# Optimization experiments

Measured on AMD Instinct MI355X. Metric: run time of the kernel, lower is better.

## Reference

```python
import jax, jax.numpy as jnp
import numpy as np

C = 512
GROUPS = 8
EPS = 1e-5


def setup_inputs() -> dict:
    key = jax.random.key(0)
    ks = jax.random.split(key, 7)
    b, c, h, w = 32, C, 32, 32
    x = jax.random.normal(ks[0], (b, c, h, w), dtype=jnp.float32)
    norm_gamma = jnp.ones((c,), dtype=jnp.float32)
    norm_beta = jnp.zeros((c,), dtype=jnp.float32)
    # 1x1 convs == per-pixel linear layers; store as [out, in] matrices
    qkv_w = jax.random.normal(ks[1], (3 * c, c), dtype=jnp.float32) * (1.0 / np.sqrt(c))
    qkv_b = jnp.zeros((3 * c,), dtype=jnp.float32)
    out_w = jax.random.normal(ks[2], (c, c), dtype=jnp.float32) * (1.0 / np.sqrt(c))
    out_b = jnp.zeros((c,), dtype=jnp.float32)
    return {"x": x, "norm_gamma": norm_gamma, "norm_beta": norm_beta,
            "qkv_w": qkv_w, "qkv_b": qkv_b, "out_w": out_w, "out_b": out_b}


def group_norm(x, gamma, beta):
    b, c, h, w = x.shape
    xg = x.reshape(b, GROUPS, c // GROUPS, h, w)
    mean = jnp.mean(xg, axis=(2, 3, 4), keepdims=True)
    var = jnp.var(xg, axis=(2, 3, 4), keepdims=True)
    xg = (xg - mean) * jax.lax.rsqrt(var + EPS)
    x = xg.reshape(b, c, h, w)
    return x * gamma[None, :, None, None] + beta[None, :, None, None]


def reference(x, norm_gamma, norm_beta, qkv_w, qkv_b, out_w, out_b):
    b, c, h, w = x.shape
    xn = group_norm(x, norm_gamma, norm_beta)
    # 1x1 conv: [b,c,h,w] -> [b,3c,h,w]
    qkv = jnp.einsum('oc,bchw->bohw', qkv_w, xn) + qkv_b[None, :, None, None]
    q, k, v = jnp.split(qkv.reshape(b, 3 * c, h * w), 3, axis=1)  # each [b,c,hw]
    scale = c ** (-0.5)
    attn = jnp.einsum('bci,bcj->bij', q, k) * scale  # [b, hw, hw]
    attn = jax.nn.softmax(attn, axis=-1)
    out = jnp.einsum('bij,bcj->bci', attn, v).reshape(b, c, h, w)
    out = jnp.einsum('oc,bchw->bohw', out_w, out) + out_b[None, :, None, None]
    return x + out
```

## Files before the change

### kernel.cpp

```cpp
#include <hip/hip_runtime.h>

#define HW 1024
#define CD 512

typedef __bf16 bf16x8 __attribute__((ext_vector_type(8)));
typedef float f32x4 __attribute__((ext_vector_type(4)));

__device__ __forceinline__ unsigned short f2bf(float f) {
    unsigned int u = __float_as_uint(f);
    u += 0x7fff + ((u >> 16) & 1);
    return (unsigned short)(u >> 16);
}
__device__ __forceinline__ float bf2f(unsigned short h) {
    return __uint_as_float((unsigned)h << 16);
}

#define AS1(p) ((__attribute__((address_space(1))) void*)(p))
#define AS3(p) ((__attribute__((address_space(3))) void*)(p))
#define GLD16(gp, lp) __builtin_amdgcn_global_load_lds(AS1(gp), AS3(lp), 16, 0, 0)
#define WAITVM(n) do { asm volatile("s_waitcnt vmcnt(" #n ")" ::: "memory"); \
                       __builtin_amdgcn_sched_barrier(0); } while (0)

__global__ __launch_bounds__(256)
void gn_stats(const float* __restrict__ x, float* __restrict__ mean, float* __restrict__ rstd) {
    int bg = blockIdx.x;
    const float4* p4 = (const float4*)(x + (size_t)bg * 65536);
    int tid = threadIdx.x;
    float s = 0.f, ss = 0.f;
#pragma unroll 8
    for (int it = 0; it < 64; ++it) {
        float4 v = p4[tid + it * 256];
        s  += v.x + v.y + v.z + v.w;
        ss += v.x * v.x + v.y * v.y + v.z * v.z + v.w * v.w;
    }
#pragma unroll
    for (int d = 32; d > 0; d >>= 1) { s += __shfl_down(s, d); ss += __shfl_down(ss, d); }
    __shared__ float ls[4], lss[4];
    if ((tid & 63) == 0) { ls[tid >> 6] = s; lss[tid >> 6] = ss; }
    __syncthreads();
    if (tid == 0) {
        float S = ls[0] + ls[1] + ls[2] + ls[3];
        float SS = lss[0] + lss[1] + lss[2] + lss[3];
        float m = S * (1.f / 65536.f);
        float v = SS * (1.f / 65536.f) - m * m;
        mean[bg] = m;
        rstd[bg] = rsqrtf(v + 1e-5f);
    }
}

__global__ __launch_bounds__(256)
void gn_norm_t(const float* __restrict__ x, const float* __restrict__ mean, const float* __restrict__ rstd,
               const float* __restrict__ gamma, const float* __restrict__ beta,
               unsigned short* __restrict__ xnT) {
    __shared__ unsigned short tile[64][67];
    int i0 = blockIdx.x * 64, c0 = blockIdx.y * 64, b = blockIdx.z;
    float m = mean[b * 8 + blockIdx.y];
    float r = rstd[b * 8 + blockIdx.y];
    int tid = threadIdx.x;
    int tr = tid >> 4, tc = (tid & 15) * 4;
    const float* xb = x + ((size_t)b * CD + c0) * HW + i0;
#pragma unroll
    for (int p = 0; p < 4; ++p) {
        int c = tr + p * 16;
        float g = gamma[c0 + c] * r;
        float bb = beta[c0 + c] - m * g;
        float4 v = *(const float4*)(xb + (size_t)c * HW + tc);
        tile[c][tc + 0] = f2bf(v.x * g + bb);
        tile[c][tc + 1] = f2bf(v.y * g + bb);
        tile[c][tc + 2] = f2bf(v.z * g + bb);
        tile[c][tc + 3] = f2bf(v.w * g + bb);
    }
    __syncthreads();
    unsigned short* ob = xnT + ((size_t)b * HW + i0) * CD + c0;
#pragma unroll
    for (int p = 0; p < 4; ++p) {
        int ir = tr + p * 16;
        ushort4 u;
        u.x = tile[tc + 0][ir];
        u.y = tile[tc + 1][ir];
        u.z = tile[tc + 2][ir];
        u.w = tile[tc + 3][ir];
        *(ushort4*)(ob + (size_t)ir * CD + tc) = u;
    }
}

__global__ __launch_bounds__(256)
void tpose3_bf16(const float* __restrict__ qkv_w, unsigned short* __restrict__ dst0) {
    __shared__ unsigned short tile[64][67];
    const int zmap[3] = {0, 2, 1};
    const float* src = qkv_w + (size_t)blockIdx.z * CD * CD;
    unsigned short* dst = dst0 + (size_t)zmap[blockIdx.z] * CD * CD;
    int i0 = blockIdx.x * 64, c0 = blockIdx.y * 64;
    int tid = threadIdx.x;
    int tr = tid >> 4, tc = (tid & 15) * 4;
#pragma unroll
    for (int p = 0; p < 4; ++p) {
        int r = tr + p * 16;
        float4 v = *(const float4*)(src + (size_t)(i0 + r) * CD + c0 + tc);
        tile[r][tc + 0] = f2bf(v.x);
        tile[r][tc + 1] = f2bf(v.y);
        tile[r][tc + 2] = f2bf(v.z);
        tile[r][tc + 3] = f2bf(v.w);
    }
    __syncthreads();
#pragma unroll
    for (int p = 0; p < 4; ++p) {
        int ir = tr + p * 16;
        ushort4 u;
        u.x = tile[tc + 0][ir];
        u.y = tile[tc + 1][ir];
        u.z = tile[tc + 2][ir];
        u.w = tile[tc + 3][ir];
        *(ushort4*)(dst + (size_t)(c0 + ir) * CD + i0 + tc) = u;
    }
}

__global__ __launch_bounds__(256)
void cvt_bf16(const float* __restrict__ src, unsigned short* __restrict__ dst) {
    int i = blockIdx.x * 256 + threadIdx.x;
    float4 v = ((const float4*)src)[i];
    ushort4 u;
    u.x = f2bf(v.x); u.y = f2bf(v.y); u.z = f2bf(v.z); u.w = f2bf(v.w);
    ((ushort4*)dst)[i] = u;
}

__global__ __launch_bounds__(256)
void gvec_kernel(const float* __restrict__ wk, const float* __restrict__ bq,
                 float* __restrict__ g) {
    __shared__ float red[4][64];
    int d = blockIdx.x * 64 + (threadIdx.x & 63);
    int os = threadIdx.x >> 6;
    float acc = 0.f;
    for (int o = os * 128; o < os * 128 + 128; ++o)
        acc += wk[(size_t)o * CD + d] * bq[o];
    red[os][threadIdx.x & 63] = acc;
    __syncthreads();
    if (threadIdx.x < 64)
        g[blockIdx.x * 64 + threadIdx.x] = red[0][threadIdx.x] + red[1][threadIdx.x] +
                                           red[2][threadIdx.x] + red[3][threadIdx.x];
}

__global__ __launch_bounds__(256)
void bias2_kernel(const float* __restrict__ out_w, const float* __restrict__ bv,
                  float* __restrict__ bias2) {
    int wid = threadIdx.x >> 6, lane = threadIdx.x & 63;
    int o = blockIdx.x * 4 + wid;
    float acc = 0.f;
#pragma unroll
    for (int t = 0; t < 512; t += 64)
        acc += out_w[(size_t)o * CD + t + lane] * bv[t + lane];
#pragma unroll
    for (int d = 32; d > 0; d >>= 1) acc += __shfl_down(acc, d);
    if (lane == 0) bias2[o] = acc;
}

template<int EPI>
__global__ __launch_bounds__(512, 2)
void gemm8(const unsigned short* __restrict__ A, const unsigned short* __restrict__ B,
           unsigned short* __restrict__ C, const float* __restrict__ bias,
           int M, int N, int K, long long sA, long long sB, long long sC) {
    unsigned nx = gridDim.x, ny = gridDim.y;
    unsigned lin = blockIdx.x + nx * (blockIdx.y + ny * blockIdx.z);
    unsigned nwg = nx * ny * gridDim.z;
    unsigned work = (lin & 7) * (nwg >> 3) + (lin >> 3);
    unsigned bx = work % nx; work /= nx;
    unsigned by = work % ny;
    unsigned bz = work / ny;

    A += (size_t)bz * sA;
    B += (size_t)bz * sB;
    int m0 = by * 256, n0 = bx * 256;

    __shared__ unsigned short lA[2][256 * 64];
    __shared__ unsigned short lB[2][256 * 64];

    int tid = threadIdx.x, lane = tid & 63, wid = tid >> 6;
    int wr = wid >> 2, wc = wid & 3;

    f32x4 acc[8][4] = {};

    int strow[4], stcol[4];
#pragma unroll
    for (int s = 0; s < 4; ++s) {
        int idx = s * 512 + tid;
        strow[s] = idx >> 3;
        stcol[s] = ((idx & 7) ^ (strow[s] & 7)) * 8;
    }

    auto stage = [&](int buf, int kt) {
        int k0 = kt << 6;
#pragma unroll
        for (int s = 0; s < 4; ++s)
            GLD16(A + (size_t)(m0 + strow[s]) * K + k0 + stcol[s], &lA[buf][(size_t)(s * 512 + tid) * 8]);
#pragma unroll
        for (int s = 0; s < 4; ++s)
            GLD16(B + (size_t)(n0 + strow[s]) * K + k0 + stcol[s], &lB[buf][(size_t)(s * 512 + tid) * 8]);
    };

    int NT = K >> 6;
    stage(0, 0);
    if (NT > 1) stage(1, 1);

    for (int t = 0; t < NT; ++t) {
        if (t < NT - 1) WAITVM(8); else WAITVM(0);
        __builtin_amdgcn_s_barrier();
        const char* pa = (const char*)lA[t & 1];
        const char* pb = (const char*)lB[t & 1];
        __builtin_amdgcn_s_setprio(1);
#pragma unroll
        for (int kk = 0; kk < 64; kk += 32) {
            int koff = (kk + (lane >> 4) * 8) * 2;
            bf16x8 af[8], bfr[4];
#pragma unroll
            for (int m = 0; m < 8; ++m) {
                int row = wr * 128 + m * 16 + (lane & 15);
                af[m] = *(const bf16x8*)(pa + ((row * 128 + koff) ^ ((row & 7) << 4)));
            }
#pragma unroll
            for (int n = 0; n < 4; ++n) {
                int row = wc * 64 + n * 16 + (lane & 15);
                bfr[n] = *(const bf16x8*)(pb + ((row * 128 + koff) ^ ((row & 7) << 4)));
            }
#pragma unroll
            for (int m = 0; m < 8; ++m)
#pragma unroll
                for (int n = 0; n < 4; ++n)
                    acc[m][n] = __builtin_amdgcn_mfma_f32_16x16x32_bf16(af[m], bfr[n], acc[m][n], 0, 0, 0);
        }
        __builtin_amdgcn_s_setprio(0);
        __builtin_amdgcn_s_barrier();
        if (t + 2 < NT) stage(t & 1, t + 2);
    }

    int rl = (lane >> 4) * 4;
    int cl = lane & 15;
    unsigned short* Cb = C + (size_t)bz * sC;
#pragma unroll
    for (int m = 0; m < 8; ++m)
#pragma unroll
        for (int n = 0; n < 4; ++n) {
            int gm = m0 + wr * 128 + m * 16 + rl;
            int gn = n0 + wc * 64 + n * 16 + cl;
#pragma unroll
            for (int rg = 0; rg < 4; ++rg) {
                float v = acc[m][n][rg];
                if (EPI == 0) v += bias[gn];
                if (EPI == 1) v += bias[gm + rg];
                Cb[(size_t)(gm + rg) * N + gn] = f2bf(v);
            }
        }
}

__global__ __launch_bounds__(512, 2)
void scores8(const unsigned short* __restrict__ T1, const unsigned short* __restrict__ xnT,
             unsigned short* __restrict__ S, float* __restrict__ tmax, float* __restrict__ tsum) {
    unsigned nx = gridDim.x, ny = gridDim.y;
    unsigned lin = blockIdx.x + nx * (blockIdx.y + ny * blockIdx.z);
    unsigned nwg = nx * ny * gridDim.z;
    unsigned work = (lin & 7) * (nwg >> 3) + (lin >> 3);
    unsigned bx = work % nx; work /= nx;
    unsigned by = work % ny;
    unsigned bz = work / ny;

    const unsigned short* Ab = T1 + (size_t)bz * HW * CD;
    const unsigned short* Bb = xnT + (size_t)bz * HW * CD;
    int m0 = by * 256, n0 = bx * 256;

    __shared__ unsigned short lA[2][256 * 64];
    __shared__ unsigned short lB[2][256 * 64];
    __shared__ float redm[4][256];
    __shared__ float reds[4][256];

    int tid = threadIdx.x, lane = tid & 63, wid = tid >> 6;
    int wr = wid >> 2, wc = wid & 3;

    f32x4 acc[8][4] = {};

    int strow[4], stcol[4];
#pragma unroll
    for (int s = 0; s < 4; ++s) {
        int idx = s * 512 + tid;
        strow[s] = idx >> 3;
        stcol[s] = ((idx & 7) ^ (strow[s] & 7)) * 8;
    }

    auto stage = [&](int buf, int kt) {
        int k0 = kt << 6;
#pragma unroll
        for (int s = 0; s < 4; ++s)
            GLD16(Ab + (size_t)(m0 + strow[s]) * CD + k0 + stcol[s], &lA[buf][(size_t)(s * 512 + tid) * 8]);
#pragma unroll
        for (int s = 0; s < 4; ++s)
            GLD16(Bb + (size_t)(n0 + strow[s]) * CD + k0 + stcol[s], &lB[buf][(size_t)(s * 512 + tid) * 8]);
    };

    stage(0, 0);
    stage(1, 1);

    for (int t = 0; t < 8; ++t) {
        if (t < 7) WAITVM(8); else WAITVM(0);
        __builtin_amdgcn_s_barrier();
        const char* pa = (const char*)lA[t & 1];
        const char* pb = (const char*)lB[t & 1];
        __builtin_amdgcn_s_setprio(1);
#pragma unroll
        for (int kk = 0; kk < 64; kk += 32) {
            int koff = (kk + (lane >> 4) * 8) * 2;
            bf16x8 af[8], bfr[4];
#pragma unroll
            for (int m = 0; m < 8; ++m) {
                int row = wr * 128 + m * 16 + (lane & 15);
                af[m] = *(const bf16x8*)(pa + ((row * 128 + koff) ^ ((row & 7) << 4)));
            }
#pragma unroll
            for (int n = 0; n < 4; ++n) {
                int row = wc * 64 + n * 16 + (lane & 15);
                bfr[n] = *(const bf16x8*)(pb + ((row * 128 + koff) ^ ((row & 7) << 4)));
            }
#pragma unroll
            for (int m = 0; m < 8; ++m)
#pragma unroll
                for (int n = 0; n < 4; ++n)
                    acc[m][n] = __builtin_amdgcn_mfma_f32_16x16x32_bf16(af[m], bfr[n], acc[m][n], 0, 0, 0);
        }
        __builtin_amdgcn_s_setprio(0);
        __builtin_amdgcn_s_barrier();
        if (t + 2 < 8) stage(t & 1, t + 2);
    }

    const float SL2E = 0.044194173824159216f * 1.4426950408889634f;
#pragma unroll
    for (int m = 0; m < 8; ++m)
#pragma unroll
        for (int n = 0; n < 4; ++n) acc[m][n] *= SL2E;

    int rl = (lane >> 4) * 4;
    int cl = lane & 15;

    float mr[8][4];
#pragma unroll
    for (int m = 0; m < 8; ++m)
#pragma unroll
        for (int rg = 0; rg < 4; ++rg)
            mr[m][rg] = fmaxf(fmaxf(acc[m][0][rg], acc[m][1][rg]),
                              fmaxf(acc[m][2][rg], acc[m][3][rg]));
#pragma unroll
    for (int d = 1; d < 16; d <<= 1)
#pragma unroll
        for (int m = 0; m < 8; ++m)
#pragma unroll
            for (int rg = 0; rg < 4; ++rg) mr[m][rg] = fmaxf(mr[m][rg], __shfl_xor(mr[m][rg], d));
    if ((lane & 15) == 0)
#pragma unroll
        for (int m = 0; m < 8; ++m)
#pragma unroll
            for (int rg = 0; rg < 4; ++rg) redm[wc][wr * 128 + m * 16 + rl + rg] = mr[m][rg];
    __syncthreads();
    float Mt[8][4];
#pragma unroll
    for (int m = 0; m < 8; ++m)
#pragma unroll
        for (int rg = 0; rg < 4; ++rg) {
            int row = wr * 128 + m * 16 + rl + rg;
            Mt[m][rg] = fmaxf(fmaxf(redm[0][row], redm[1][row]),
                              fmaxf(redm[2][row], redm[3][row]));
        }

    float sr[8][4] = {};
#pragma unroll
    for (int m = 0; m < 8; ++m)
#pragma unroll
        for (int n = 0; n < 4; ++n)
#pragma unroll
            for (int rg = 0; rg < 4; ++rg) {
                float e = __builtin_amdgcn_exp2f(acc[m][n][rg] - Mt[m][rg]);
                acc[m][n][rg] = e;
                sr[m][rg] += e;
            }
#pragma unroll
    for (int d = 1; d < 16; d <<= 1)
#pragma unroll
        for (int m = 0; m < 8; ++m)
#pragma unroll
            for (int rg = 0; rg < 4; ++rg) sr[m][rg] += __shfl_xor(sr[m][rg], d);
    if ((lane & 15) == 0)
#pragma unroll
        for (int m = 0; m < 8; ++m)
#pragma unroll
            for (int rg = 0; rg < 4; ++rg) reds[wc][wr * 128 + m * 16 + rl + rg] = sr[m][rg];
    __syncthreads();

    if (tid < 256) {
        float M = fmaxf(fmaxf(redm[0][tid], redm[1][tid]),
                        fmaxf(redm[2][tid], redm[3][tid]));
        float Z = reds[0][tid] + reds[1][tid] + reds[2][tid] + reds[3][tid];
        size_t o = ((size_t)bz * 4 + bx) * HW + m0 + tid;
        tmax[o] = M;
        tsum[o] = Z;
    }

    unsigned short* Sb = S + (size_t)bz * HW * HW;
#pragma unroll
    for (int m = 0; m < 8; ++m)
#pragma unroll
        for (int n = 0; n < 4; ++n) {
            int gm = m0 + wr * 128 + m * 16 + rl;
            int gn = n0 + wc * 64 + n * 16 + cl;
#pragma unroll
            for (int rg = 0; rg < 4; ++rg)
                Sb[(size_t)(gm + rg) * HW + gn] = f2bf(acc[m][n][rg]);
        }
}

template<int EPI>
__global__ __launch_bounds__(256, 2)
void gemm_bt(const unsigned short* __restrict__ A, const unsigned short* __restrict__ B,
             void* __restrict__ Cv, const float* __restrict__ bias,
             int M, int N, int K, long long sA, long long sB, long long sC) {
    unsigned nx = gridDim.x, ny = gridDim.y;
    unsigned lin = blockIdx.x + nx * (blockIdx.y + ny * blockIdx.z);
    unsigned nwg = nx * ny * gridDim.z;
    unsigned work = (lin & 7) * (nwg >> 3) + (lin >> 3);
    unsigned bx = work % nx; work /= nx;
    unsigned by = work % ny;
    unsigned bz = work / ny;

    A += (size_t)bz * sA;
    B += (size_t)bz * sB;
    int m0 = by * 128, n0 = bx * 128;

    __shared__ unsigned short lA[2][128 * 64];
    __shared__ unsigned short lB[2][128 * 64];

    int tid = threadIdx.x;
    int lane = tid & 63;
    int wr = (tid >> 6) >> 1, wc = (tid >> 6) & 1;

    f32x4 acc[4][4] = {};

    int strow[4], stcol[4];
#pragma unroll
    for (int s = 0; s < 4; ++s) {
        int row = (s * 256 + tid) >> 3;
        int g = (tid & 7) ^ (row & 7);
        strow[s] = row;
        stcol[s] = g * 8;
    }

    auto stage = [&](int buf, int k0) {
#pragma unroll
        for (int s = 0; s < 4; ++s) {
            GLD16(A + (size_t)(m0 + strow[s]) * K + k0 + stcol[s], &lA[buf][(size_t)(s * 256 + tid) * 8]);
            GLD16(B + (size_t)(n0 + strow[s]) * K + k0 + stcol[s], &lB[buf][(size_t)(s * 256 + tid) * 8]);
        }
    };

    int NT = K >> 6;
    stage(0, 0);
    __syncthreads();
    int cur = 0;
    for (int t = 0; t < NT; ++t) {
        if (t + 1 < NT) stage(cur ^ 1, (t + 1) << 6);
        const char* pa = (const char*)lA[cur];
        const char* pb = (const char*)lB[cur];
#pragma unroll
        for (int kk = 0; kk < 64; kk += 32) {
            bf16x8 af[4], bfr[4];
#pragma unroll
            for (int m = 0; m < 4; ++m) {
                int row = wr * 64 + m * 16 + (lane & 15);
                int off = (row * 128 + (kk + (lane >> 4) * 8) * 2) ^ ((row & 7) << 4);
                af[m] = *(const bf16x8*)(pa + off);
            }
#pragma unroll
            for (int n = 0; n < 4; ++n) {
                int row = wc * 64 + n * 16 + (lane & 15);
                int off = (row * 128 + (kk + (lane >> 4) * 8) * 2) ^ ((row & 7) << 4);
                bfr[n] = *(const bf16x8*)(pb + off);
            }
#pragma unroll
            for (int m = 0; m < 4; ++m)
#pragma unroll
                for (int n = 0; n < 4; ++n)
                    acc[m][n] = __builtin_amdgcn_mfma_f32_16x16x32_bf16(af[m], bfr[n], acc[m][n], 0, 0, 0);
        }
        __syncthreads();
        cur ^= 1;
    }

    int rl = (lane >> 4) * 4;
    int cl = lane & 15;
    unsigned short* Cb = (unsigned short*)Cv + (size_t)bz * sC;
#pragma unroll
    for (int m = 0; m < 4; ++m)
#pragma unroll
        for (int n = 0; n < 4; ++n) {
            int gm = m0 + wr * 64 + m * 16 + rl;
            int gn = n0 + wc * 64 + n * 16 + cl;
#pragma unroll
            for (int rg = 0; rg < 4; ++rg) {
                float v = acc[m][n][rg];
                if (EPI == 0) v += bias[gn];
                if (EPI == 1) v += bias[gm + rg];
                Cb[(size_t)(gm + rg) * N + gn] = f2bf(v);
            }
        }
}

__global__ __launch_bounds__(256)
void rescale_kernel(const float* __restrict__ tmax, const float* __restrict__ tsum,
                    float* __restrict__ ratio) {
    int r = blockIdx.x * 256 + threadIdx.x;
    int b = r >> 10, i = r & 1023;
    const float* tm = tmax + (size_t)b * 4 * HW + i;
    const float* ts = tsum + (size_t)b * 4 * HW + i;
    float M = -1e30f;
#pragma unroll
    for (int jt = 0; jt < 4; ++jt) M = fmaxf(M, tm[(size_t)jt * HW]);
    float Z = 0.f;
#pragma unroll
    for (int jt = 0; jt < 4; ++jt) Z += ts[(size_t)jt * HW] * __builtin_amdgcn_exp2f(tm[(size_t)jt * HW] - M);
    float rZ = 1.0f / Z;
#pragma unroll
    for (int jt = 0; jt < 3; ++jt)
        ratio[((size_t)b * 4 + jt) * HW + i] =
            __builtin_amdgcn_exp2f(tm[(size_t)jt * HW] - tm[(size_t)(jt + 1) * HW]);
    ratio[((size_t)b * 4 + 3) * HW + i] = __builtin_amdgcn_exp2f(tm[(size_t)3 * HW] - M) * rZ;
}

__global__ __launch_bounds__(256)
void pv_gemm(const unsigned short* __restrict__ A, const unsigned short* __restrict__ B,
             float* __restrict__ C, const float* __restrict__ bias,
             const float* __restrict__ resid, const float* __restrict__ ratio) {
    unsigned nx = gridDim.x, ny = gridDim.y;
    unsigned lin = blockIdx.x + nx * (blockIdx.y + ny * blockIdx.z);
    unsigned nwg = nx * ny * gridDim.z;
    unsigned work = (lin & 7) * (nwg >> 3) + (lin >> 3);
    unsigned bx = work % nx; work /= nx;
    unsigned by = work % ny;
    unsigned bz = work / ny;

    A += (size_t)bz * 512 * 1024;
    B += (size_t)bz * 1024 * 1024;
    int m0 = by * 128, n0 = bx * 128;

    __shared__ unsigned short lA[2][128 * 64];
    __shared__ unsigned short lB[2][128 * 64];

    int tid = threadIdx.x, lane = tid & 63;
    int wr = (tid >> 6) >> 1, wc = (tid >> 6) & 1;
    int cl = lane & 15;

    f32x4 acc[4][4] = {};

    int strow[4], stcol[4];
#pragma unroll
    for (int s = 0; s < 4; ++s) {
        int row = (s * 256 + tid) >> 3;
        int g = (tid & 7) ^ (row & 7);
        strow[s] = row;
        stcol[s] = g * 8;
    }

    auto stage = [&](int buf, int k0) {
#pragma unroll
        for (int s = 0; s < 4; ++s) {
            GLD16(A + (size_t)(m0 + strow[s]) * 1024 + k0 + stcol[s], &lA[buf][(size_t)(s * 256 + tid) * 8]);
            GLD16(B + (size_t)(n0 + strow[s]) * 1024 + k0 + stcol[s], &lB[buf][(size_t)(s * 256 + tid) * 8]);
        }
    };

    const float* rbase = ratio + (size_t)bz * 4 * HW + n0 + wc * 64 + cl;

    stage(0, 0);
    __syncthreads();
    int cur = 0;
    float r0 = 0.f, r1 = 0.f, r2 = 0.f, r3 = 0.f;
    for (int t = 0; t < 16; ++t) {
        if (t + 1 < 16) stage(cur ^ 1, (t + 1) << 6);
        if (!(t & 3)) {
            int jt = t >> 2;
            r0 = rbase[(size_t)jt * HW + 0];
            r1 = rbase[(size_t)jt * HW + 16];
            r2 = rbase[(size_t)jt * HW + 32];
            r3 = rbase[(size_t)jt * HW + 48];
        }
        const char* pa = (const char*)lA[cur];
        const char* pb = (const char*)lB[cur];
#pragma unroll
        for (int kk = 0; kk < 64; kk += 32) {
            bf16x8 af[4], bfr[4];
#pragma unroll
            for (int m = 0; m < 4; ++m) {
                int row = wr * 64 + m * 16 + (lane & 15);
                int off = (row * 128 + (kk + (lane >> 4) * 8) * 2) ^ ((row & 7) << 4);
                af[m] = *(const bf16x8*)(pa + off);
            }
#pragma unroll
            for (int n = 0; n < 4; ++n) {
                int row = wc * 64 + n * 16 + (lane & 15);
                int off = (row * 128 + (kk + (lane >> 4) * 8) * 2) ^ ((row & 7) << 4);
                bfr[n] = *(const bf16x8*)(pb + off);
            }
#pragma unroll
            for (int m = 0; m < 4; ++m)
#pragma unroll
                for (int n = 0; n < 4; ++n)
                    acc[m][n] = __builtin_amdgcn_mfma_f32_16x16x32_bf16(af[m], bfr[n], acc[m][n], 0, 0, 0);
        }
        __syncthreads();
        cur ^= 1;
        if ((t & 3) == 3) {
#pragma unroll
            for (int m = 0; m < 4; ++m) {
                acc[m][0] *= r0;
                acc[m][1] *= r1;
                acc[m][2] *= r2;
                acc[m][3] *= r3;
            }
        }
    }

    int rl = (lane >> 4) * 4;
    float* Cf = C + (size_t)bz * 512 * 1024;
    const float* Rs = resid + (size_t)bz * 512 * 1024;
#pragma unroll
    for (int m = 0; m < 4; ++m)
#pragma unroll
        for (int n = 0; n < 4; ++n) {
            int gm = m0 + wr * 64 + m * 16 + rl;
            int gn = n0 + wc * 64 + n * 16 + cl;
#pragma unroll
            for (int rg = 0; rg < 4; ++rg) {
                size_t off = (size_t)(gm + rg) * 1024 + gn;
                Cf[off] = acc[m][n][rg] + bias[gm + rg] + Rs[off];
            }
        }
}

extern "C" void kernel_launch(void* const* d_in, const int* in_sizes, int n_in,
                              void* d_out, int out_size, void* d_ws, size_t ws_size,
                              hipStream_t stream) {
    const float* x      = (const float*)d_in[0];
    const float* gamma  = (const float*)d_in[1];
    const float* beta   = (const float*)d_in[2];
    const float* qkv_w  = (const float*)d_in[3];
    const float* qkv_b  = (const float*)d_in[4];
    const float* out_w  = (const float*)d_in[5];
    const float* out_b  = (const float*)d_in[6];

    char* ws = (char*)d_ws;
    unsigned short* xnT  = (unsigned short*)ws;
    unsigned short* vpr  = (unsigned short*)(ws + 33554432);
    unsigned short* SP   = (unsigned short*)(ws + 67108864);
    unsigned short* wqkT = (unsigned short*)(ws + 100663296);
    unsigned short* w2   = (unsigned short*)(ws + 101187584);
    float* gvec          = (float*)(ws + 101711872);
    float* bias2         = (float*)(ws + 101713920);
    float* meanp         = (float*)(ws + 101715968);
    float* rstdp         = (float*)(ws + 101716992);
    float* tmaxp         = (float*)(ws + 101718016);
    float* tsump         = (float*)(ws + 102766592);
    float* ratiop        = (float*)(ws + 103815168);

    unsigned short* slot0 = SP;
    unsigned short* owb   = SP + 786432;

    unsigned short* T1 = (unsigned short*)((char*)d_out + 33554432);
    float* outF = (float*)d_out;

    const float* wk_f = qkv_w + (size_t)512 * CD;

    gn_stats<<<256, 256, 0, stream>>>(x, meanp, rstdp);
    gn_norm_t<<<dim3(16, 8, 32), 256, 0, stream>>>(x, meanp, rstdp, gamma, beta, xnT);

    tpose3_bf16<<<dim3(8, 8, 3), 256, 0, stream>>>(qkv_w, slot0);
    cvt_bf16<<<256, 256, 0, stream>>>(out_w, owb);
    gvec_kernel<<<8, 256, 0, stream>>>(wk_f, qkv_b, gvec);
    bias2_kernel<<<128, 256, 0, stream>>>(out_w, qkv_b + 1024, bias2);

    gemm_bt<3><<<dim3(4, 4, 2), 256, 0, stream>>>(slot0 + 524288, slot0, wqkT, nullptr,
        512, 512, 512, 262144, 262144, 262144);

    gemm8<0><<<dim3(2, 4, 32), 512, 0, stream>>>(xnT, wqkT, T1, gvec,
        1024, 512, 512, 1024LL * 512, 0, 1024LL * 512);
    gemm8<1><<<dim3(4, 2, 32), 512, 0, stream>>>(w2, xnT, vpr, bias2,
        512, 1024, 512, 0, 1024LL * 512, 512LL * 1024);

    for (int h = 0; h < 2; ++h) {
        const unsigned short* T1h = T1 + (size_t)h * 16 * 1024 * 512;
        const unsigned short* xh  = xnT + (size_t)h * 16 * 1024 * 512;
        float* tmaxh = tmaxp + (size_t)h * 16 * 4 * 1024;
        float* tsumh = tsump + (size_t)h * 16 * 4 * 1024;

        scores8<<<dim3(4, 4, 16), 512, 0, stream>>>(T1h, xh, SP, tmaxh, tsumh);
        rescale_kernel<<<64, 256, 0, stream>>>(tmaxh, tsumh, ratiop);
        pv_gemm<<<dim3(8, 4, 16), 256, 0, stream>>>(
            vpr + (size_t)h * 16 * 512 * 1024, SP,
            outF + (size_t)h * 16 * 512 * 1024, out_b,
            x + (size_t)h * 16 * 512 * 1024, ratiop);
    }
    (void)in_sizes; (void)n_in; (void)out_size; (void)ws_size;
}
```

Measured before the change: 218.5 us.

## Deepen GEMM load pipeline with counted vmcnt waits and preloaded ratios

Restructures the output-projection GEMM main loop so two K-tiles are in flight: it issues stages for tiles 0 and 1 up front and waits with explicit vmcnt counts instead of a full __syncthreads drain. It also hoists all rescaling-ratio loads before the loop and raises wave priority around the MFMA block. The goal is to hide global-to-LDS load latency better and remove per-iteration full syncs. In exchange it uses more registers for the ratios and depends on hand-counted vmcnt values being correct.

```diff
diff --git a/kernel.cpp b/kernel.cpp
--- a/kernel.cpp
+++ b/kernel.cpp
@@ -562,7 +562,18 @@
         stcol[s] = g * 8;
     }
 
-    auto stage = [&](int buf, int k0) {
+    const float* rbase = ratio + (size_t)bz * 4 * HW + n0 + wc * 64 + cl;
+    float rv[4][4];
+#pragma unroll
+    for (int jt = 0; jt < 4; ++jt) {
+        rv[jt][0] = rbase[(size_t)jt * HW + 0];
+        rv[jt][1] = rbase[(size_t)jt * HW + 16];
+        rv[jt][2] = rbase[(size_t)jt * HW + 32];
+        rv[jt][3] = rbase[(size_t)jt * HW + 48];
+    }
+
+    auto stage = [&](int buf, int kt) {
+        int k0 = kt << 6;
 #pragma unroll
         for (int s = 0; s < 4; ++s) {
             GLD16(A + (size_t)(m0 + strow[s]) * 1024 + k0 + stcol[s], &lA[buf][(size_t)(s * 256 + tid) * 8]);
@@ -570,37 +581,31 @@
         }
     };
 
-    const float* rbase = ratio + (size_t)bz * 4 * HW + n0 + wc * 64 + cl;
+    asm volatile("s_waitcnt vmcnt(0)" ::: "memory");
+    __builtin_amdgcn_sched_barrier(0);
 
     stage(0, 0);
-    __syncthreads();
-    int cur = 0;
-    float r0 = 0.f, r1 = 0.f, r2 = 0.f, r3 = 0.f;
+    stage(1, 1);
+
     for (int t = 0; t < 16; ++t) {
-        if (t + 1 < 16) stage(cur ^ 1, (t + 1) << 6);
-        if (!(t & 3)) {
-            int jt = t >> 2;
-            r0 = rbase[(size_t)jt * HW + 0];
-            r1 = rbase[(size_t)jt * HW + 16];
-            r2 = rbase[(size_t)jt * HW + 32];
-            r3 = rbase[(size_t)jt * HW + 48];
-        }
-        const char* pa = (const char*)lA[cur];
-        const char* pb = (const char*)lB[cur];
+        if (t < 15) WAITVM(8); else WAITVM(0);
+        __builtin_amdgcn_s_barrier();
+        const char* pa = (const char*)lA[t & 1];
+        const char* pb = (const char*)lB[t & 1];
+        __builtin_amdgcn_s_setprio(1);
 #pragma unroll
         for (int kk = 0; kk < 64; kk += 32) {
+            int koff = (kk + (lane >> 4) * 8) * 2;
             bf16x8 af[4], bfr[4];
 #pragma unroll
             for (int m = 0; m < 4; ++m) {
                 int row = wr * 64 + m * 16 + (lane & 15);
-                int off = (row * 128 + (kk + (lane >> 4) * 8) * 2) ^ ((row & 7) << 4);
-                af[m] = *(const bf16x8*)(pa + off);
+                af[m] = *(const bf16x8*)(pa + ((row * 128 + koff) ^ ((row & 7) << 4)));
             }
 #pragma unroll
             for (int n = 0; n < 4; ++n) {
                 int row = wc * 64 + n * 16 + (lane & 15);
-                int off = (row * 128 + (kk + (lane >> 4) * 8) * 2) ^ ((row & 7) << 4);
-                bfr[n] = *(const bf16x8*)(pb + off);
+                bfr[n] = *(const bf16x8*)(pb + ((row * 128 + koff) ^ ((row & 7) << 4)));
             }
 #pragma unroll
             for (int m = 0; m < 4; ++m)
@@ -608,15 +613,17 @@
                 for (int n = 0; n < 4; ++n)
                     acc[m][n] = __builtin_amdgcn_mfma_f32_16x16x32_bf16(af[m], bfr[n], acc[m][n], 0, 0, 0);
         }
-        __syncthreads();
-        cur ^= 1;
+        __builtin_amdgcn_s_setprio(0);
+        __builtin_amdgcn_s_barrier();
+        if (t + 2 < 16) stage(t & 1, t + 2);
         if ((t & 3) == 3) {
+            int jt = t >> 2;
 #pragma unroll
             for (int m = 0; m < 4; ++m) {
-                acc[m][0] *= r0;
-                acc[m][1] *= r1;
-                acc[m][2] *= r2;
-                acc[m][3] *= r3;
+                acc[m][0] *= rv[jt][0];
+                acc[m][1] *= rv[jt][1];
+                acc[m][2] *= rv[jt][2];
+                acc[m][3] *= rv[jt][3];
             }
         }
     }
```

New measurement: 221.5 us. Within noise of the previous version (+1.3%).
